# Kernel tuning notes

Hardware: AMD Instinct MI355X
Metric: run time of the kernel (lower is better)

## Reference

```python
import jax, jax.numpy as jnp
import numpy as np

N_HEADS = 4
D_K = 64

def setup_inputs() -> dict:
    key = jax.random.key(0)
    k1, k2, k3 = jax.random.split(key, 3)
    B, C, H, W = 16, 256, 32, 32
    x = jax.random.normal(k1, (B, C, H, W), dtype=jnp.float32)
    # Linear(C, 3*n_heads*d_k) stored as [in, out] for x @ W
    w_proj = jax.random.normal(k2, (C, 3 * N_HEADS * D_K), dtype=jnp.float32) * (1.0 / np.sqrt(C))
    b_proj = jnp.zeros((3 * N_HEADS * D_K,), dtype=jnp.float32)
    w_out = jax.random.normal(k3, (N_HEADS * D_K, C), dtype=jnp.float32) * (1.0 / np.sqrt(N_HEADS * D_K))
    b_out = jnp.zeros((C,), dtype=jnp.float32)
    return {"x": x, "w_proj": w_proj, "b_proj": b_proj, "w_out": w_out, "b_out": b_out}

def reference(x, w_proj, b_proj, w_out, b_out):
    B, C, H, W = x.shape
    S = H * W
    scale = D_K ** -0.5
    xs = x.reshape(B, C, S).transpose(0, 2, 1)            # [B, S, C]
    qkv = (xs @ w_proj + b_proj).reshape(B, S, N_HEADS, 3 * D_K)
    q, k, v = jnp.split(qkv, 3, axis=3)                    # each [B, S, H, dk]
    attn = jnp.einsum('bihd,bjhd->bijh', q, k) * scale     # [B, S, S, heads]
    attn = jax.nn.softmax(attn, axis=2)
    o = jnp.einsum('bijh,bjhd->bihd', attn, v)             # [B, S, heads, dk]
    o = o.reshape(B, S, N_HEADS * D_K)
    res = o @ w_out + b_out + xs                           # [B, S, C]
    return res.transpose(0, 2, 1).reshape(B, C, H, W)
```

## Files before the change

### kernel.cpp

```cpp
#include <hip/hip_runtime.h>
#include <math.h>

#define B_  16
#define C_  256
#define S_  1024
#define NH  4
#define DK  64
#define P3  768
#define ND  256

typedef unsigned short u16;
typedef unsigned int   u32;
typedef float  f32x4  __attribute__((ext_vector_type(4)));
typedef short  bf16x8 __attribute__((ext_vector_type(8)));

#define MFMA16(a, b, c) __builtin_amdgcn_mfma_f32_16x16x32_bf16(a, b, c, 0, 0, 0)

#define QSCALE 0.1803368801111137f

#define WAITVM(N) asm volatile("s_waitcnt vmcnt(" #N ")" ::: "memory")
#define BARRIER() asm volatile("s_barrier" ::: "memory")

__device__ __forceinline__ u16 f2bf(float f) {
    union { float f; u32 u; } x; x.f = f;
    u32 r = x.u + 0x7fffu + ((x.u >> 16) & 1u);
    return (u16)(r >> 16);
}

__device__ __forceinline__ u32 cvtpk(float lo, float hi) {
    u32 r;
    asm("v_cvt_pk_bf16_f32 %0, %1, %2" : "=v"(r) : "v"(lo), "v"(hi));
    return r;
}

__device__ __forceinline__ void stage16(const u16* g, u16* l) {
    __builtin_amdgcn_global_load_lds(
        (const __attribute__((address_space(1))) void*)g,
        (__attribute__((address_space(3))) void*)l, 16, 0, 0);
}

__global__ __launch_bounds__(256) void transpose_all(
    const float* __restrict__ x, u16* __restrict__ xt,
    const float* __restrict__ wp, u16* __restrict__ wpT,
    const float* __restrict__ wo, u16* __restrict__ woT)
{
    const int z = blockIdx.z;
    const float* src;
    u16* dst;
    int Cc;
    if (z < 16)       { src = x + (size_t)z * C_ * S_; dst = xt + (size_t)z * C_ * S_; Cc = S_; }
    else if (z == 16) { src = wp; dst = wpT; Cc = P3; }
    else              { src = wo; dst = woT; Cc = ND; }
    if ((int)blockIdx.x * 64 >= Cc) return;
    const int R = C_;

    __shared__ float T[64][65];
    const int tid = threadIdx.x;
    const int c0 = blockIdx.x * 64, r0 = blockIdx.y * 64;

    const int l64 = tid & 63, rr0 = tid >> 6;
    #pragma unroll
    for (int t = 0; t < 16; ++t) {
        int rr = rr0 + t * 4;
        T[rr][l64] = src[(size_t)(r0 + rr) * Cc + c0 + l64];
    }
    __syncthreads();
    const int rp = tid & 31;
    const int cb = tid >> 5;
    #pragma unroll
    for (int t = 0; t < 8; ++t) {
        int c = cb + t * 8;
        u32 lo = f2bf(T[2 * rp][c]);
        u32 hi = f2bf(T[2 * rp + 1][c]);
        *(u32*)&dst[(size_t)(c0 + c) * R + r0 + 2 * rp] = lo | (hi << 16);
    }
}

__global__ __launch_bounds__(256) void qkv_mfma(
    const u16* __restrict__ xt, const u16* __restrict__ wpT,
    const float* __restrict__ bp, u16* __restrict__ qo,
    u16* __restrict__ ko, u16* __restrict__ vo)
{
    __shared__ __align__(16) u16 SM[24576];

    const int tid = threadIdx.x;
    const int w = tid >> 6, lane = tid & 63;
    const int n_ = lane & 15, quad = lane >> 4;
    const int n0 = blockIdx.x * 64, s0 = blockIdx.y * 128, b = blockIdx.z;

    const u16* ar0 = xt + ((size_t)b * S_ + s0 + (2 * w + 0) * 16 + n_) * C_ + quad * 8;
    const u16* ar1 = xt + ((size_t)b * S_ + s0 + (2 * w + 1) * 16 + n_) * C_ + quad * 8;
    const u16* br  = wpT + (size_t)(n0 + w * 16 + n_) * C_ + quad * 8;

    f32x4 acc[2][4];
    #pragma unroll
    for (int am = 0; am < 2; ++am)
        #pragma unroll
        for (int nf = 0; nf < 4; ++nf)
            #pragma unroll
            for (int r = 0; r < 4; ++r) acc[am][nf][r] = 0.f;

    {
        u16* As_ = SM;
        u16* Bs_ = SM + 8192;
        stage16(ar0,      As_ + (4 * w + 0) * 512);
        stage16(ar0 + 32, As_ + (4 * w + 1) * 512);
        stage16(ar1,      As_ + (4 * w + 2) * 512);
        stage16(ar1 + 32, As_ + (4 * w + 3) * 512);
        stage16(br,       Bs_ + (2 * w + 0) * 512);
        stage16(br + 32,  Bs_ + (2 * w + 1) * 512);
    }

    #pragma unroll
    for (int p = 0; p < 4; ++p) {
        u16* As_ = SM + (p & 1) * 12288;
        u16* Bs_ = As_ + 8192;
        if (p < 3) {
            const int pk = (p + 1) * 64;
            u16* An = SM + ((p + 1) & 1) * 12288;
            u16* Bn = An + 8192;
            stage16(ar0 + pk,      An + (4 * w + 0) * 512);
            stage16(ar0 + pk + 32, An + (4 * w + 1) * 512);
            stage16(ar1 + pk,      An + (4 * w + 2) * 512);
            stage16(ar1 + pk + 32, An + (4 * w + 3) * 512);
            stage16(br  + pk,      Bn + (2 * w + 0) * 512);
            stage16(br  + pk + 32, Bn + (2 * w + 1) * 512);
            WAITVM(6);
        } else {
            WAITVM(0);
        }
        BARRIER();
        #pragma unroll
        for (int kc = 0; kc < 2; ++kc) {
            bf16x8 af0 = *(const bf16x8*)&As_[((2 * w + 0) * 2 + kc) * 512 + lane * 8];
            bf16x8 af1 = *(const bf16x8*)&As_[((2 * w + 1) * 2 + kc) * 512 + lane * 8];
            #pragma unroll
            for (int nf = 0; nf < 4; ++nf) {
                bf16x8 bf = *(const bf16x8*)&Bs_[(nf * 2 + kc) * 512 + lane * 8];
                acc[0][nf] = MFMA16(af0, bf, acc[0][nf]);
                acc[1][nf] = MFMA16(af1, bf, acc[1][nf]);
            }
        }
        if (p < 3) BARRIER();
    }

    const int hd = n0 / 192, rem = n0 % 192, which = rem / 64;
    const int bh = b * NH + hd;
    float bias[4];
    #pragma unroll
    for (int nf = 0; nf < 4; ++nf) bias[nf] = bp[n0 + nf * 16 + n_];
    const float sc = (which == 0) ? QSCALE : 1.f;

    __syncthreads();
    if (which < 2) {
        u16* Cs = SM;
        #pragma unroll
        for (int am = 0; am < 2; ++am) {
            int row0 = w * 32 + am * 16 + quad * 4;
            #pragma unroll
            for (int nf = 0; nf < 4; ++nf)
                #pragma unroll
                for (int r = 0; r < 4; ++r)
                    Cs[(row0 + r) * 72 + nf * 16 + n_] =
                        f2bf((acc[am][nf][r] + bias[nf]) * sc);
        }
        __syncthreads();
        u16* dst = (which == 0) ? qo : ko;
        #pragma unroll
        for (int t = 0; t < 4; ++t) {
            int ii = tid + t * 256;
            int row = ii >> 3, c8 = (ii & 7) * 8;
            *(bf16x8*)&dst[((size_t)bh * S_ + s0 + row) * DK + c8] =
                *(const bf16x8*)&Cs[row * 72 + c8];
        }
    } else {
        u16* Cs = SM;
        #pragma unroll
        for (int am = 0; am < 2; ++am) {
            int colb = w * 32 + am * 16 + quad * 4;
            #pragma unroll
            for (int nf = 0; nf < 4; ++nf)
                #pragma unroll
                for (int r = 0; r < 4; ++r)
                    Cs[(nf * 16 + n_) * 136 + colb + r] =
                        f2bf(acc[am][nf][r] + bias[nf]);
        }
        __syncthreads();
        #pragma unroll
        for (int t = 0; t < 4; ++t) {
            int ii = tid + t * 256;
            int row = ii >> 4, c8 = (ii & 15) * 8;
            *(bf16x8*)&vo[((size_t)bh * DK + row) * S_ + s0 + c8] =
                *(const bf16x8*)&Cs[row * 136 + c8];
        }
    }
}

__global__ __launch_bounds__(256) void attn_mfma(
    const u16* __restrict__ q, const u16* __restrict__ k,
    const u16* __restrict__ vt, u16* __restrict__ obf)
{
    __shared__ __align__(16) u16 SM[32768];

    const int tid = threadIdx.x;
    const int w = tid >> 6, lane = tid & 63;
    const int n_ = lane & 15, quad = lane >> 4;

    const int id  = blockIdx.x;
    const int nid = (id & 7) * 64 + (id >> 3);
    const int i0  = (nid & 7) * 128;
    const int bh  = nid >> 3;
    const int hd  = bh & 3;
    const int b   = bh >> 2;

    bf16x8 qf[2][2];
    #pragma unroll
    for (int am = 0; am < 2; ++am) {
        const u16* qrow = q + ((size_t)bh * S_ + i0 + w * 32 + am * 16 + n_) * DK;
        qf[am][0] = *(const bf16x8*)&qrow[quad * 8];
        qf[am][1] = *(const bf16x8*)&qrow[32 + quad * 8];
    }

    const int kappa = 32 * (w & 1) + 8 * (n_ >> 2) + 4 * (w >> 1) + (n_ & 3);
    const u16* kbase = k  + ((size_t)bh * S_ + kappa) * DK + quad * 8;
    const u16* vbase = vt + ((size_t)bh * DK + w * 16 + n_) * S_ + quad * 8;

    float lsum[2] = {0.f, 0.f};
    f32x4 oacc[2][4];
    #pragma unroll
    for (int am = 0; am < 2; ++am)
        #pragma unroll
        for (int nd = 0; nd < 4; ++nd)
            #pragma unroll
            for (int r = 0; r < 4; ++r) oacc[am][nd][r] = 0.f;

    stage16(kbase,                SM + w * 1024);
    stage16(kbase + 32,           SM + w * 1024 + 512);
    stage16(vbase,                SM + 4096 + w * 1024);
    stage16(vbase + 32,           SM + 4096 + w * 1024 + 512);
    stage16(kbase + 64 * DK,      SM + 8192 + w * 1024);
    stage16(kbase + 64 * DK + 32, SM + 8192 + w * 1024 + 512);
    stage16(vbase + 64,           SM + 8192 + 4096 + w * 1024);
    stage16(vbase + 64 + 32,      SM + 8192 + 4096 + w * 1024 + 512);

    for (int t = 0; t < 16; ++t) {
        u16* Ks = SM + (t & 3) * 8192;
        u16* Vs = Ks + 4096;
        if (t < 14) {
            const size_t jn = (size_t)(t + 2) * 64;
            u16* Kn = SM + ((t + 2) & 3) * 8192;
            u16* Vn = Kn + 4096;
            stage16(kbase + jn * DK,      Kn + w * 1024);
            stage16(kbase + jn * DK + 32, Kn + w * 1024 + 512);
            stage16(vbase + jn,           Vn + w * 1024);
            stage16(vbase + jn + 32,      Vn + w * 1024 + 512);
            WAITVM(8);
        } else if (t == 14) {
            WAITVM(4);
        } else {
            WAITVM(0);
        }
        BARRIER();

        f32x4 sb[2][4];
        __builtin_amdgcn_s_setprio(1);
        #pragma unroll
        for (int nb = 0; nb < 4; ++nb) {
            bf16x8 kf0 = *(const bf16x8*)&Ks[nb * 1024 + lane * 8];
            bf16x8 kf1 = *(const bf16x8*)&Ks[nb * 1024 + 512 + lane * 8];
            #pragma unroll
            for (int am = 0; am < 2; ++am) {
                f32x4 a; a[0] = a[1] = a[2] = a[3] = 0.f;
                a = MFMA16(kf0, qf[am][0], a);
                a = MFMA16(kf1, qf[am][1], a);
                sb[am][nb] = a;
            }
        }
        __builtin_amdgcn_s_setprio(0);

        bf16x8 pa[2][2];
        #pragma unroll
        for (int am = 0; am < 2; ++am) {
            float pr[4][4];
            #pragma unroll
            for (int nb = 0; nb < 4; ++nb)
                #pragma unroll
                for (int r = 0; r < 4; ++r) {
                    float p = exp2f(sb[am][nb][r]);
                    lsum[am] += p;
                    pr[nb][r] = p;
                }
            union { bf16x8 v; u32 u[4]; } p0, p1;
            p0.u[0] = cvtpk(pr[0][0], pr[0][1]);
            p0.u[1] = cvtpk(pr[0][2], pr[0][3]);
            p0.u[2] = cvtpk(pr[2][0], pr[2][1]);
            p0.u[3] = cvtpk(pr[2][2], pr[2][3]);
            p1.u[0] = cvtpk(pr[1][0], pr[1][1]);
            p1.u[1] = cvtpk(pr[1][2], pr[1][3]);
            p1.u[2] = cvtpk(pr[3][0], pr[3][1]);
            p1.u[3] = cvtpk(pr[3][2], pr[3][3]);
            pa[am][0] = p0.v;
            pa[am][1] = p1.v;
        }

        __builtin_amdgcn_s_setprio(1);
        #pragma unroll
        for (int nd = 0; nd < 4; ++nd) {
            bf16x8 vf0 = *(const bf16x8*)&Vs[nd * 1024 + lane * 8];
            bf16x8 vf1 = *(const bf16x8*)&Vs[nd * 1024 + 512 + lane * 8];
            #pragma unroll
            for (int am = 0; am < 2; ++am) {
                oacc[am][nd] = MFMA16(vf0, pa[am][0], oacc[am][nd]);
                oacc[am][nd] = MFMA16(vf1, pa[am][1], oacc[am][nd]);
            }
        }
        __builtin_amdgcn_s_setprio(0);
    }

    float inv[2];
    #pragma unroll
    for (int am = 0; am < 2; ++am) {
        float s = lsum[am];
        s += __shfl_xor(s, 16);
        s += __shfl_xor(s, 32);
        inv[am] = 1.f / s;
    }

    __syncthreads();
    u16* eb = SM + w * 2304;
    #pragma unroll
    for (int am = 0; am < 2; ++am)
        #pragma unroll
        for (int nd = 0; nd < 4; ++nd) {
            uint2 uv;
            uv.x = cvtpk(oacc[am][nd][0] * inv[am], oacc[am][nd][1] * inv[am]);
            uv.y = cvtpk(oacc[am][nd][2] * inv[am], oacc[am][nd][3] * inv[am]);
            *(uint2*)&eb[(am * 16 + n_) * 72 + nd * 16 + quad * 4] = uv;
        }
    __syncthreads();
    #pragma unroll
    for (int t = 0; t < 4; ++t) {
        int ii = lane + t * 64;
        int row = ii >> 3, c8 = (ii & 7) * 8;
        *(bf16x8*)&obf[((size_t)b * S_ + i0 + w * 32 + row) * ND + hd * DK + c8] =
            *(const bf16x8*)&eb[row * 72 + c8];
    }
}

__global__ __launch_bounds__(256) void out_proj_mfma(
    const u16* __restrict__ obf, const u16* __restrict__ woT,
    const float* __restrict__ bo, const float* __restrict__ x,
    float* __restrict__ out)
{
    __shared__ __align__(16) u16 SM[24576];

    const int tid = threadIdx.x;
    const int w = tid >> 6, lane = tid & 63;
    const int n_ = lane & 15, quad = lane >> 4;
    const int c0 = blockIdx.x * 64, s0 = blockIdx.y * 128, b = blockIdx.z;

    const u16* ar  = woT + (size_t)(c0 + w * 16 + n_) * ND + quad * 8;
    const u16* br0 = obf + ((size_t)b * S_ + s0 + (2 * w + 0) * 16 + n_) * ND + quad * 8;
    const u16* br1 = obf + ((size_t)b * S_ + s0 + (2 * w + 1) * 16 + n_) * ND + quad * 8;

    f32x4 acc[2][4];
    #pragma unroll
    for (int nf = 0; nf < 2; ++nf)
        #pragma unroll
        for (int mb = 0; mb < 4; ++mb)
            #pragma unroll
            for (int r = 0; r < 4; ++r) acc[nf][mb][r] = 0.f;

    {
        u16* Bs_ = SM;
        u16* As_ = SM + 8192;
        stage16(br0,      Bs_ + (4 * w + 0) * 512);
        stage16(br0 + 32, Bs_ + (4 * w + 1) * 512);
        stage16(br1,      Bs_ + (4 * w + 2) * 512);
        stage16(br1 + 32, Bs_ + (4 * w + 3) * 512);
        stage16(ar,       As_ + (2 * w + 0) * 512);
        stage16(ar + 32,  As_ + (2 * w + 1) * 512);
    }

    #pragma unroll
    for (int p = 0; p < 4; ++p) {
        u16* Bs_ = SM + (p & 1) * 12288;
        u16* As_ = Bs_ + 8192;
        if (p < 3) {
            const int pk = (p + 1) * 64;
            u16* Bn = SM + ((p + 1) & 1) * 12288;
            u16* An = Bn + 8192;
            stage16(br0 + pk,      Bn + (4 * w + 0) * 512);
            stage16(br0 + pk + 32, Bn + (4 * w + 1) * 512);
            stage16(br1 + pk,      Bn + (4 * w + 2) * 512);
            stage16(br1 + pk + 32, Bn + (4 * w + 3) * 512);
            stage16(ar  + pk,      An + (2 * w + 0) * 512);
            stage16(ar  + pk + 32, An + (2 * w + 1) * 512);
            WAITVM(6);
        } else {
            WAITVM(0);
        }
        BARRIER();
        #pragma unroll
        for (int kc = 0; kc < 2; ++kc) {
            bf16x8 bf0 = *(const bf16x8*)&Bs_[((2 * w + 0) * 2 + kc) * 512 + lane * 8];
            bf16x8 bf1 = *(const bf16x8*)&Bs_[((2 * w + 1) * 2 + kc) * 512 + lane * 8];
            #pragma unroll
            for (int mb = 0; mb < 4; ++mb) {
                bf16x8 af = *(const bf16x8*)&As_[(mb * 2 + kc) * 512 + lane * 8];
                acc[0][mb] = MFMA16(af, bf0, acc[0][mb]);
                acc[1][mb] = MFMA16(af, bf1, acc[1][mb]);
            }
        }
        if (p < 3) BARRIER();
    }

    #pragma unroll
    for (int mb = 0; mb < 4; ++mb)
        #pragma unroll
        for (int r = 0; r < 4; ++r) {
            int c = c0 + mb * 16 + quad * 4 + r;
            float bias = bo[c];
            #pragma unroll
            for (int nf = 0; nf < 2; ++nf) {
                size_t idx = ((size_t)b * C_ + c) * S_ + s0 + w * 32 + nf * 16 + n_;
                out[idx] = acc[nf][mb][r] + bias + x[idx];
            }
        }
}

extern "C" void kernel_launch(void* const* d_in, const int* in_sizes, int n_in,
                              void* d_out, int out_size, void* d_ws, size_t ws_size,
                              hipStream_t stream) {
    const float* x  = (const float*)d_in[0];
    const float* wp = (const float*)d_in[1];
    const float* bp = (const float*)d_in[2];
    const float* wo = (const float*)d_in[3];
    const float* bo = (const float*)d_in[4];
    float* out = (float*)d_out;

    const size_t QKV_E = (size_t)B_ * NH * S_ * DK;
    u16* q   = (u16*)d_ws;
    u16* kk  = q   + QKV_E;
    u16* vtp = kk  + QKV_E;
    u16* obf = vtp + QKV_E;
    u16* xt  = obf + (size_t)B_ * S_ * ND;
    u16* wpT = xt  + (size_t)B_ * S_ * C_;
    u16* woT = wpT + (size_t)P3 * C_;

    transpose_all<<<dim3(16, 4, 18),             256, 0, stream>>>(x, xt, wp, wpT, wo, woT);
    qkv_mfma     <<<dim3(P3 / 64, S_ / 128, B_), 256, 0, stream>>>(xt, wpT, bp, q, kk, vtp);
    attn_mfma    <<<dim3(512, 1, 1),             256, 0, stream>>>(q, kk, vtp, obf);
    out_proj_mfma<<<dim3(C_ / 64, S_ / 128, B_), 256, 0, stream>>>(obf, woT, bo, x, out);
}
```

Baseline: 139.9 us.

## Software-pipeline PV MFMA one tile behind QK and compute row sums via MFMA

Restructures the attention loop so the P·V MFMAs for the previous key tile run right after the current tile's QK^T MFMAs, hiding exp latency behind matrix work. The per-element scalar row-sum accumulation and the cross-lane shuffles are replaced by extra MFMAs against a ones vector. It also switches to the raw exp2 builtin and moves the wait and barrier to the top of the iteration. In exchange it adds MFMA work and register pressure, and changes LDS buffer lifetimes, which risks races on the 4-slot ring.

```diff
diff --git a/kernel.cpp b/kernel.cpp
--- a/kernel.cpp
+++ b/kernel.cpp
@@ -20,6 +20,12 @@
 
 #define WAITVM(N) asm volatile("s_waitcnt vmcnt(" #N ")" ::: "memory")
 #define BARRIER() asm volatile("s_barrier" ::: "memory")
+
+#if __has_builtin(__builtin_amdgcn_exp2f)
+#define EXP2F(x) __builtin_amdgcn_exp2f(x)
+#else
+#define EXP2F(x) exp2f(x)
+#endif
 
 __device__ __forceinline__ u16 f2bf(float f) {
     union { float f; u32 u; } x; x.f = f;
@@ -221,18 +227,26 @@
         qf[am][1] = *(const bf16x8*)&qrow[32 + quad * 8];
     }
 
+    union { bf16x8 v; u32 u[4]; } ones_;
+    #pragma unroll
+    for (int i = 0; i < 4; ++i) ones_.u[i] = 0x3F803F80u;
+    const bf16x8 onesf = ones_.v;
+
     const int kappa = 32 * (w & 1) + 8 * (n_ >> 2) + 4 * (w >> 1) + (n_ & 3);
     const u16* kbase = k  + ((size_t)bh * S_ + kappa) * DK + quad * 8;
     const u16* vbase = vt + ((size_t)bh * DK + w * 16 + n_) * S_ + quad * 8;
 
-    float lsum[2] = {0.f, 0.f};
     f32x4 oacc[2][4];
-    #pragma unroll
-    for (int am = 0; am < 2; ++am)
+    f32x4 acc_sum[2];
+    #pragma unroll
+    for (int am = 0; am < 2; ++am) {
         #pragma unroll
         for (int nd = 0; nd < 4; ++nd)
             #pragma unroll
             for (int r = 0; r < 4; ++r) oacc[am][nd][r] = 0.f;
+        #pragma unroll
+        for (int r = 0; r < 4; ++r) acc_sum[am][r] = 0.f;
+    }
 
     stage16(kbase,                SM + w * 1024);
     stage16(kbase + 32,           SM + w * 1024 + 512);
@@ -243,9 +257,13 @@
     stage16(vbase + 64,           SM + 8192 + 4096 + w * 1024);
     stage16(vbase + 64 + 32,      SM + 8192 + 4096 + w * 1024 + 512);
 
+    bf16x8 pa[2][2];
+
     for (int t = 0; t < 16; ++t) {
         u16* Ks = SM + (t & 3) * 8192;
-        u16* Vs = Ks + 4096;
+        u16* Vp = SM + ((t + 3) & 3) * 8192 + 4096;
+        if (t < 15) WAITVM(4); else WAITVM(0);
+        BARRIER();
         if (t < 14) {
             const size_t jn = (size_t)(t + 2) * 64;
             u16* Kn = SM + ((t + 2) & 3) * 8192;
@@ -254,13 +272,7 @@
             stage16(kbase + jn * DK + 32, Kn + w * 1024 + 512);
             stage16(vbase + jn,           Vn + w * 1024);
             stage16(vbase + jn + 32,      Vn + w * 1024 + 512);
-            WAITVM(8);
-        } else if (t == 14) {
-            WAITVM(4);
-        } else {
-            WAITVM(0);
-        }
-        BARRIER();
+        }
 
         f32x4 sb[2][4];
         __builtin_amdgcn_s_setprio(1);
@@ -276,20 +288,34 @@
                 sb[am][nb] = a;
             }
         }
+
+        if (t > 0) {
+            #pragma unroll
+            for (int nd = 0; nd < 4; ++nd) {
+                bf16x8 vf0 = *(const bf16x8*)&Vp[nd * 1024 + lane * 8];
+                bf16x8 vf1 = *(const bf16x8*)&Vp[nd * 1024 + 512 + lane * 8];
+                #pragma unroll
+                for (int am = 0; am < 2; ++am) {
+                    oacc[am][nd] = MFMA16(vf0, pa[am][0], oacc[am][nd]);
+                    oacc[am][nd] = MFMA16(vf1, pa[am][1], oacc[am][nd]);
+                }
+            }
+            #pragma unroll
+            for (int am = 0; am < 2; ++am) {
+                acc_sum[am] = MFMA16(onesf, pa[am][0], acc_sum[am]);
+                acc_sum[am] = MFMA16(onesf, pa[am][1], acc_sum[am]);
+            }
+        }
         __builtin_amdgcn_s_setprio(0);
 
-        bf16x8 pa[2][2];
         #pragma unroll
         for (int am = 0; am < 2; ++am) {
             float pr[4][4];
             #pragma unroll
             for (int nb = 0; nb < 4; ++nb)
                 #pragma unroll
-                for (int r = 0; r < 4; ++r) {
-                    float p = exp2f(sb[am][nb][r]);
-                    lsum[am] += p;
-                    pr[nb][r] = p;
-                }
+                for (int r = 0; r < 4; ++r)
+                    pr[nb][r] = EXP2F(sb[am][nb][r]);
             union { bf16x8 v; u32 u[4]; } p0, p1;
             p0.u[0] = cvtpk(pr[0][0], pr[0][1]);
             p0.u[1] = cvtpk(pr[0][2], pr[0][3]);
@@ -302,29 +328,32 @@
             pa[am][0] = p0.v;
             pa[am][1] = p1.v;
         }
-
+    }
+
+    {
+        u16* Vp = SM + 3 * 8192 + 4096;
         __builtin_amdgcn_s_setprio(1);
         #pragma unroll
         for (int nd = 0; nd < 4; ++nd) {
-            bf16x8 vf0 = *(const bf16x8*)&Vs[nd * 1024 + lane * 8];
-            bf16x8 vf1 = *(const bf16x8*)&Vs[nd * 1024 + 512 + lane * 8];
+            bf16x8 vf0 = *(const bf16x8*)&Vp[nd * 1024 + lane * 8];
+            bf16x8 vf1 = *(const bf16x8*)&Vp[nd * 1024 + 512 + lane * 8];
             #pragma unroll
             for (int am = 0; am < 2; ++am) {
                 oacc[am][nd] = MFMA16(vf0, pa[am][0], oacc[am][nd]);
                 oacc[am][nd] = MFMA16(vf1, pa[am][1], oacc[am][nd]);
             }
         }
+        #pragma unroll
+        for (int am = 0; am < 2; ++am) {
+            acc_sum[am] = MFMA16(onesf, pa[am][0], acc_sum[am]);
+            acc_sum[am] = MFMA16(onesf, pa[am][1], acc_sum[am]);
+        }
         __builtin_amdgcn_s_setprio(0);
     }
 
-    float inv[2];
-    #pragma unroll
-    for (int am = 0; am < 2; ++am) {
-        float s = lsum[am];
-        s += __shfl_xor(s, 16);
-        s += __shfl_xor(s, 32);
-        inv[am] = 1.f / s;
-    }
+    const float inv0 = 1.f / acc_sum[0][0];
+    const float inv1 = 1.f / acc_sum[1][0];
+    float inv[2] = {inv0, inv1};
 
     __syncthreads();
     u16* eb = SM + w * 2304;
```

Measured after the change: 128.8 us. -8.0%, faster.
